# Performance work log

Hardware: AMD Instinct MI355X
Metric: run time of the kernel (lower is better)

The kernel has to match this reference:

```python
import jax, jax.numpy as jnp
import numpy as np

IN_DIMS = [16, 16, 16]
OUT_DIMS = [16, 16, 16]
RANKS = [1, 16, 16, 1]
BATCH = 1024


def setup_inputs() -> dict:
    key = jax.random.key(0)
    ks = jax.random.split(key, 1 + len(IN_DIMS))
    vector = jax.random.normal(ks[0], (BATCH, *IN_DIMS), dtype=jnp.float32)
    inp = {"vector": vector}
    for i in range(len(IN_DIMS)):
        shape = (RANKS[i], OUT_DIMS[i], IN_DIMS[i], RANKS[i + 1])
        scale = 1.0 / float(np.sqrt(RANKS[i] * IN_DIMS[i]))
        inp[f"core{i}"] = jax.random.normal(ks[1 + i], shape, dtype=jnp.float32) * scale
    return inp


def _tt_matvec(vector, cores):
    """y = M @ x where M is the TT/MPO matrix defined by `cores`.

    vector: (B, d_in_1, ..., d_in_d). Returns (B, d_out_1, ..., d_out_d).
    Mirrors TTMatrix.metric_projection exactly (output dims absorbed into batch).
    """
    bs0 = vector.shape[0]
    res = vector[:, None]  # (B, r0=1, d_in_1, ..., d_in_d)
    bs = bs0
    for core in cores:
        r, o, i, k = core.shape
        rem = res.shape[3:]  # remaining un-contracted input dims
        res_t = res.reshape(bs, r, i, -1)  # (bs, r, i, x)
        # contract rank-in and input dim: (r,o,i,k),(b,r,i,x) -> (b,k,o,x)
        new = jnp.einsum('roik,brix->bkox', core, res_t)
        new = jnp.transpose(new, (0, 2, 1, 3)).reshape(bs * o, k, *rem)
        bs = bs * o
        res = new
    res = jnp.squeeze(res, axis=-1)  # last rank is 1
    out_dims = [c.shape[1] for c in cores]
    return res.reshape(bs0, *out_dims)


def reference(vector, core0, core1, core2):
    return _tt_matvec(vector, (core0, core1, core2))
```

## Files before the change

kernel.cpp:

```cpp
#include <hip/hip_runtime.h>
#include <hip/hip_bf16.h>


typedef short bf16x8 __attribute__((ext_vector_type(8)));
typedef float f32x4 __attribute__((ext_vector_type(4)));

#define WS_A1_OFF 0
#define WS_A0_OFF 131072
#define WS_A2_OFF 147456
#define WS_NEEDED 155648

__device__ __forceinline__ unsigned short f2bf(float f) {
    union { float f; unsigned int u; } x; x.f = f;
    unsigned int u = x.u;
    u += 0x7fffu + ((u >> 16) & 1u);
    return (unsigned short)(u >> 16);
}

__device__ __forceinline__ unsigned int pk_bf16(float lo, float hi) {
    __hip_bfloat162 h = __float22bfloat162_rn(make_float2(lo, hi));
    unsigned int r;
    __builtin_memcpy(&r, &h, 4);
    return r;
}

__global__ void tt_repack(const float* __restrict__ c0,
                          const float* __restrict__ c1,
                          const float* __restrict__ c2,
                          unsigned short* __restrict__ ws) {
    int idx = blockIdx.x * 256 + threadIdx.x;
    if (idx < 8192) {
        int o2 = idx >> 9, ks = (idx >> 6) & 7, l = idx & 63;
        int k2 = l & 15;
        unsigned short* dst = ws + ((size_t)(o2 * 8 + ks) * 64 + l) * 8;
        #pragma unroll
        for (int j = 0; j < 8; ++j) {
            int k = ks * 32 + ((l >> 4) * 8) + j;
            dst[j] = f2bf(c1[(k & 15) * 4096 + o2 * 256 + (k >> 4) * 16 + k2]);
        }
    } else if (idx < 9216) {
        int t = idx - 8192;
        int o1 = t >> 6, l = t & 63;
        unsigned short* dst = ws + WS_A0_OFF / 2 + ((size_t)o1 * 64 + l) * 8;
        #pragma unroll
        for (int j = 0; j < 8; ++j) {
            int k = ((l >> 4) * 8) + j;
            float v = (l < 32) ? c0[o1 * 256 + k * 16 + (l & 15)] : 0.f;
            dst[j] = f2bf(v);
        }
    } else if (idx < 9728) {
        int t = idx - 9216;
        int ks = t >> 6, l = t & 63;
        unsigned short* dst = ws + WS_A2_OFF / 2 + ((size_t)ks * 64 + l) * 8;
        #pragma unroll
        for (int j = 0; j < 8; ++j) {
            int k = ks * 32 + ((l >> 4) * 8) + j;
            dst[j] = f2bf(c2[(k & 15) * 256 + (l & 15) * 16 + (k >> 4)]);
        }
    }
}

template <bool PACKED>
__global__ __launch_bounds__(512, 2) void tt_main(
    const float* __restrict__ vg, const float* __restrict__ c0,
    const float* __restrict__ c1, const float* __restrict__ c2,
    const unsigned short* __restrict__ ws, float* __restrict__ outg)
{
    __shared__ unsigned short T1[16384];
    __shared__ unsigned short T2[2][16384];

    const int b   = blockIdx.x;
    const int t   = threadIdx.x;
    const int w   = t >> 6;
    const int l   = t & 63;
    const int l15 = l & 15;
    const int lg  = l >> 4;
    const int mg  = w >> 1;
    const int ng  = w & 1;

    bf16x8 fb0[2];
    {
        const float* vb = vg + (size_t)b * 4096;
        #pragma unroll
        for (int nt = 0; nt < 2; ++nt) {
            bf16x8 f = {0, 0, 0, 0, 0, 0, 0, 0};
            if (l < 32) {
                int i2 = 2 * w + nt;
                const float* p = vb + (lg * 8) * 256 + i2 * 16 + l15;
                #pragma unroll
                for (int j = 0; j < 8; ++j) f[j] = (short)f2bf(p[j * 256]);
            }
            fb0[nt] = f;
        }
    }

    bf16x8 fa1p[32];
    if constexpr (PACKED) {
        const unsigned short* a1p = ws + (size_t)l * 8;
        #pragma unroll
        for (int rt = 0; rt < 4; ++rt)
            #pragma unroll
            for (int ks = 0; ks < 8; ++ks)
                fa1p[rt * 8 + ks] = *(const bf16x8*)(a1p + ((size_t)((4 * mg + rt) * 8 + ks)) * 512);
    } else {
        for (int rt = 0; rt < 4; ++rt)
            for (int ks = 0; ks < 8; ++ks) {
                int o2 = 4 * mg + rt;
                bf16x8 f;
                for (int j = 0; j < 8; ++j) {
                    int k = ks * 32 + lg * 8 + j;
                    f[j] = (short)f2bf(c1[(k & 15) * 4096 + o2 * 256 + (k >> 4) * 16 + l15]);
                }
                fa1p[rt * 8 + ks] = f;
            }
    }

    for (int nc = 0; nc < 4; ++nc) {
        unsigned short* T2c = T2[nc & 1];

        bf16x8 fa0p[4];
        if constexpr (PACKED) {
            #pragma unroll
            for (int mtl = 0; mtl < 4; ++mtl)
                fa0p[mtl] = *(const bf16x8*)(ws + WS_A0_OFF / 2 +
                                             ((size_t)(nc * 4 + mtl) * 64 + l) * 8);
        } else {
            for (int mtl = 0; mtl < 4; ++mtl) {
                bf16x8 f = {0, 0, 0, 0, 0, 0, 0, 0};
                if (l < 32) {
                    for (int j = 0; j < 8; ++j)
                        f[j] = (short)f2bf(c0[(nc * 4 + mtl) * 256 + (lg * 8 + j) * 16 + l15]);
                }
                fa0p[mtl] = f;
            }
        }

        #pragma unroll
        for (int mtl = 0; mtl < 4; ++mtl) {
            #pragma unroll
            for (int nt = 0; nt < 2; ++nt) {
                f32x4 z = {0.f, 0.f, 0.f, 0.f};
                f32x4 d = __builtin_amdgcn_mfma_f32_16x16x32_bf16(fa0p[mtl], fb0[nt], z, 0, 0, 0);
                const int i2 = 2 * w + nt;
                const int n  = mtl * 16 + l15;
                int byte = (n * 512 + (i2 * 16 + lg * 4) * 2) ^ ((l15 & 7) << 4);
                uint2 wv;
                wv.x = pk_bf16(d[0], d[1]);
                wv.y = pk_bf16(d[2], d[3]);
                *(uint2*)((char*)T1 + byte) = wv;
            }
        }
        __syncthreads();

        {
            f32x4 acc[4][2];
            #pragma unroll
            for (int rt = 0; rt < 4; ++rt)
                #pragma unroll
                for (int ntl = 0; ntl < 2; ++ntl) acc[rt][ntl] = (f32x4){0.f, 0.f, 0.f, 0.f};

            #pragma unroll
            for (int ks = 0; ks < 8; ++ks) {
                #pragma unroll
                for (int ntl = 0; ntl < 2; ++ntl) {
                    const int nt = 2 * ng + ntl;
                    int byte = ((nt * 16 + l15) * 512 + (ks * 32 + lg * 8) * 2) ^ ((l15 & 7) << 4);
                    bf16x8 fb = *(const bf16x8*)((char*)T1 + byte);
                    acc[0][ntl] = __builtin_amdgcn_mfma_f32_16x16x32_bf16(fa1p[0 * 8 + ks], fb, acc[0][ntl], 0, 0, 0);
                    acc[1][ntl] = __builtin_amdgcn_mfma_f32_16x16x32_bf16(fa1p[1 * 8 + ks], fb, acc[1][ntl], 0, 0, 0);
                    acc[2][ntl] = __builtin_amdgcn_mfma_f32_16x16x32_bf16(fa1p[2 * 8 + ks], fb, acc[2][ntl], 0, 0, 0);
                    acc[3][ntl] = __builtin_amdgcn_mfma_f32_16x16x32_bf16(fa1p[3 * 8 + ks], fb, acc[3][ntl], 0, 0, 0);
                }
            }
            #pragma unroll
            for (int rt = 0; rt < 4; ++rt) {
                const int o2 = 4 * mg + rt;
                #pragma unroll
                for (int ntl = 0; ntl < 2; ++ntl) {
                    const int nt = 2 * ng + ntl;
                    int byte = ((nt * 16 + o2) * 512 + (l15 * 16 + lg * 4) * 2) ^ ((o2 & 7) << 4);
                    uint2 wv;
                    wv.x = pk_bf16(acc[rt][ntl][0], acc[rt][ntl][1]);
                    wv.y = pk_bf16(acc[rt][ntl][2], acc[rt][ntl][3]);
                    *(uint2*)((char*)T2c + byte) = wv;
                }
            }
        }
        __syncthreads();

        if (w < 4) {
            bf16x8 fa2[8];
            if constexpr (PACKED) {
                #pragma unroll
                for (int ks = 0; ks < 8; ++ks)
                    fa2[ks] = *(const bf16x8*)(ws + WS_A2_OFF / 2 + ((size_t)ks * 64 + l) * 8);
            } else {
                for (int ks = 0; ks < 8; ++ks) {
                    bf16x8 f;
                    for (int j = 0; j < 8; ++j) {
                        int k = ks * 32 + lg * 8 + j;
                        f[j] = (short)f2bf(c2[(k & 15) * 256 + l15 * 16 + (k >> 4)]);
                    }
                    fa2[ks] = f;
                }
            }
            f32x4 a3a = {0.f, 0.f, 0.f, 0.f};
            f32x4 a3b = {0.f, 0.f, 0.f, 0.f};
            #pragma unroll
            for (int ks = 0; ks < 8; ks += 2) {
                int byte0 = ((w * 16 + l15) * 512 + ((ks + 0) * 32 + lg * 8) * 2) ^ ((l15 & 7) << 4);
                int byte1 = ((w * 16 + l15) * 512 + ((ks + 1) * 32 + lg * 8) * 2) ^ ((l15 & 7) << 4);
                bf16x8 fbA = *(const bf16x8*)((char*)T2c + byte0);
                bf16x8 fbB = *(const bf16x8*)((char*)T2c + byte1);
                a3a = __builtin_amdgcn_mfma_f32_16x16x32_bf16(fa2[ks],     fbA, a3a, 0, 0, 0);
                a3b = __builtin_amdgcn_mfma_f32_16x16x32_bf16(fa2[ks + 1], fbB, a3b, 0, 0, 0);
            }
            f32x4 acc3 = a3a + a3b;
            float* ob = outg + (size_t)b * 4096;
            *(f32x4*)(ob + (nc * 4 + w) * 256 + l15 * 16 + lg * 4) = acc3;
        }
    }
}

extern "C" void kernel_launch(void* const* d_in, const int* in_sizes, int n_in,
                              void* d_out, int out_size, void* d_ws, size_t ws_size,
                              hipStream_t stream) {
    const float* vg  = (const float*)d_in[0];
    const float* c0g = (const float*)d_in[1];
    const float* c1g = (const float*)d_in[2];
    const float* c2g = (const float*)d_in[3];
    float* outg = (float*)d_out;

    const int B = in_sizes[0] / 4096;
    const bool packed = (ws_size >= (size_t)WS_NEEDED) && (d_ws != nullptr);

    if (packed) {
        tt_repack<<<dim3(38), dim3(256), 0, stream>>>(c0g, c1g, c2g, (unsigned short*)d_ws);
        tt_main<true><<<dim3(B), dim3(512), 0, stream>>>(
            vg, c0g, c1g, c2g, (const unsigned short*)d_ws, outg);
    } else {
        tt_main<false><<<dim3(B), dim3(512), 0, stream>>>(
            vg, c0g, c1g, c2g, nullptr, outg);
    }
}
```

Measured before the change: 57.49 us.

## Fold cores 0 and 1 into a combined weight and batch four vectors per block

Adds a new path that precomputes the product of core0 and core1 into a 256x256-per-o1 bf16 weight matrix in workspace, then a main kernel that handles four batch elements per block. It runs one large GEMM per o1 against the staged input, with the core2 contraction for the previous o1 overlapped using double-buffered shared memory. This removes the separate first-stage contraction and the per-block T1 round trip, and spreads weight loads over four batch items. In exchange it needs about 2 MB of workspace, a heavier repack kernel, more weight traffic per block from L2, and it changes bf16 rounding because the fused weights are rounded once.

```diff
diff --git a/kernel.cpp b/kernel.cpp
--- a/kernel.cpp
+++ b/kernel.cpp
@@ -9,6 +9,9 @@
 #define WS_A0_OFF 131072
 #define WS_A2_OFF 147456
 #define WS_NEEDED 155648
+#define WS2_W12_OFF 0
+#define WS2_C2_OFF  2097152
+#define WS2_NEEDED  2105344
 
 __device__ __forceinline__ unsigned short f2bf(float f) {
     union { float f; unsigned int u; } x; x.f = f;
@@ -23,6 +26,174 @@
     __builtin_memcpy(&r, &h, 4);
     return r;
 }
+
+
+__global__ void tt_repack2(const float* __restrict__ c0,
+                           const float* __restrict__ c1,
+                           const float* __restrict__ c2,
+                           unsigned short* __restrict__ ws) {
+    if (blockIdx.x < 256) {
+        int idx = blockIdx.x * 512 + threadIdx.x;
+        int mt = idx >> 9, ks = (idx >> 6) & 7, l = idx & 63;
+        int o1 = mt >> 4, o2 = mt & 15;
+        int k2 = l & 15, lg = l >> 4;
+        int i1 = 2 * ks + (lg >> 1);
+        int i2b = (lg & 1) * 8;
+        float c0row[16];
+        #pragma unroll
+        for (int k1 = 0; k1 < 16; ++k1) c0row[k1] = c0[o1 * 256 + i1 * 16 + k1];
+        unsigned short* dst = ws + ((size_t)(mt * 8 + ks) * 64 + l) * 8;
+        #pragma unroll
+        for (int j = 0; j < 8; ++j) {
+            int i2 = i2b + j;
+            float s = 0.f;
+            #pragma unroll
+            for (int k1 = 0; k1 < 16; ++k1)
+                s += c0row[k1] * c1[k1 * 4096 + o2 * 256 + i2 * 16 + k2];
+            dst[j] = f2bf(s);
+        }
+    } else {
+        int t = threadIdx.x;
+        int ks = t >> 6, l = t & 63;
+        unsigned short* dst = ws + WS2_C2_OFF / 2 + ((size_t)ks * 64 + l) * 8;
+        #pragma unroll
+        for (int j = 0; j < 8; ++j) {
+            int k = ks * 32 + ((l >> 4) * 8) + j;
+            dst[j] = f2bf(c2[(k & 15) * 256 + (l & 15) * 16 + (k >> 4)]);
+        }
+    }
+}
+
+__global__ __launch_bounds__(512, 2) void tt_main2(
+    const float* __restrict__ vg, const unsigned short* __restrict__ ws,
+    float* __restrict__ outg)
+{
+    __shared__ unsigned short vS[16384];
+    __shared__ unsigned short T2[2][16384];
+
+    const int b0  = blockIdx.x * 4;
+    const int t   = threadIdx.x;
+    const int w   = t >> 6;
+    const int l   = t & 63;
+    const int l15 = l & 15;
+    const int lg  = l >> 4;
+
+    bf16x8 fa2[8];
+    #pragma unroll
+    for (int ks = 0; ks < 8; ++ks)
+        fa2[ks] = *(const bf16x8*)(ws + WS2_C2_OFF / 2 + ((size_t)ks * 64 + l) * 8);
+
+    {
+        const int bl  = t >> 7;
+        const int i3  = (t >> 3) & 15;
+        const int i1h = t & 7;
+        const float* vb = vg + (size_t)(b0 + bl) * 4096;
+        const int rowbyte = (bl * 16 + i3) * 512;
+        const int swz = (i3 & 7) << 4;
+        #pragma unroll
+        for (int q = 0; q < 4; ++q) {
+            const int i1  = 2 * i1h + (q >> 1);
+            const int i2b = (q & 1) * 8;
+            unsigned int pk[4];
+            #pragma unroll
+            for (int p = 0; p < 4; ++p) {
+                float lo = vb[i1 * 256 + (i2b + 2 * p)     * 16 + i3];
+                float hi = vb[i1 * 256 + (i2b + 2 * p + 1) * 16 + i3];
+                pk[p] = pk_bf16(lo, hi);
+            }
+            int byte = (rowbyte + (i1 * 16 + i2b) * 2) ^ swz;
+            *(uint4*)((char*)vS + byte) = make_uint4(pk[0], pk[1], pk[2], pk[3]);
+        }
+    }
+    __syncthreads();
+
+    const int o2a = w, o2b = w + 8;
+
+    int curr = 0;
+    for (int o1 = 0; o1 < 16; ++o1) {
+        bf16x8 fA0[8], fA1[8];
+        #pragma unroll
+        for (int ks = 0; ks < 8; ++ks) {
+            fA0[ks] = *(const bf16x8*)(ws + ((size_t)((o1 * 16 + o2a) * 8 + ks) * 64 + l) * 8);
+            fA1[ks] = *(const bf16x8*)(ws + ((size_t)((o1 * 16 + o2b) * 8 + ks) * 64 + l) * 8);
+        }
+
+        if (o1 > 0 && w < 4) {
+            const unsigned short* T2p = T2[curr ^ 1];
+            f32x4 a3a = {0.f, 0.f, 0.f, 0.f};
+            f32x4 a3b = {0.f, 0.f, 0.f, 0.f};
+            #pragma unroll
+            for (int ks3 = 0; ks3 < 8; ks3 += 2) {
+                const int i3A = 2 * ks3 + (lg >> 1);
+                const int i3B = i3A + 2;
+                const int k2b = (lg & 1) * 8;
+                int byteA = ((w * 16 + i3A) * 512 + (l15 * 16 + k2b) * 2) ^ ((i3A & 7) << 4);
+                int byteB = ((w * 16 + i3B) * 512 + (l15 * 16 + k2b) * 2) ^ ((i3B & 7) << 4);
+                bf16x8 fbA = *(const bf16x8*)((char*)T2p + byteA);
+                bf16x8 fbB = *(const bf16x8*)((char*)T2p + byteB);
+                a3a = __builtin_amdgcn_mfma_f32_16x16x32_bf16(fa2[ks3],     fbA, a3a, 0, 0, 0);
+                a3b = __builtin_amdgcn_mfma_f32_16x16x32_bf16(fa2[ks3 + 1], fbB, a3b, 0, 0, 0);
+            }
+            f32x4 acc3 = a3a + a3b;
+            *(f32x4*)(outg + (size_t)(b0 + w) * 4096 + (o1 - 1) * 256 + l15 * 16 + lg * 4) = acc3;
+        }
+
+        {
+            f32x4 acc[2][4];
+            #pragma unroll
+            for (int mi = 0; mi < 2; ++mi)
+                #pragma unroll
+                for (int nt = 0; nt < 4; ++nt) acc[mi][nt] = (f32x4){0.f, 0.f, 0.f, 0.f};
+
+            #pragma unroll
+            for (int ks = 0; ks < 8; ++ks) {
+                #pragma unroll
+                for (int nt = 0; nt < 4; ++nt) {
+                    int byte = ((nt * 16 + l15) * 512 + (ks * 32 + lg * 8) * 2) ^ ((l15 & 7) << 4);
+                    bf16x8 fb = *(const bf16x8*)((char*)vS + byte);
+                    acc[0][nt] = __builtin_amdgcn_mfma_f32_16x16x32_bf16(fA0[ks], fb, acc[0][nt], 0, 0, 0);
+                    acc[1][nt] = __builtin_amdgcn_mfma_f32_16x16x32_bf16(fA1[ks], fb, acc[1][nt], 0, 0, 0);
+                }
+            }
+            unsigned short* T2c = T2[curr];
+            #pragma unroll
+            for (int mi = 0; mi < 2; ++mi) {
+                const int o2 = mi ? o2b : o2a;
+                #pragma unroll
+                for (int nt = 0; nt < 4; ++nt) {
+                    int byte = ((nt * 16 + l15) * 512 + (o2 * 16 + lg * 4) * 2) ^ ((l15 & 7) << 4);
+                    uint2 wv;
+                    wv.x = pk_bf16(acc[mi][nt][0], acc[mi][nt][1]);
+                    wv.y = pk_bf16(acc[mi][nt][2], acc[mi][nt][3]);
+                    *(uint2*)((char*)T2c + byte) = wv;
+                }
+            }
+        }
+        __syncthreads();
+        curr ^= 1;
+    }
+
+    if (w < 4) {
+        const unsigned short* T2p = T2[curr ^ 1];
+        f32x4 a3a = {0.f, 0.f, 0.f, 0.f};
+        f32x4 a3b = {0.f, 0.f, 0.f, 0.f};
+        #pragma unroll
+        for (int ks3 = 0; ks3 < 8; ks3 += 2) {
+            const int i3A = 2 * ks3 + (lg >> 1);
+            const int i3B = i3A + 2;
+            const int k2b = (lg & 1) * 8;
+            int byteA = ((w * 16 + i3A) * 512 + (l15 * 16 + k2b) * 2) ^ ((i3A & 7) << 4);
+            int byteB = ((w * 16 + i3B) * 512 + (l15 * 16 + k2b) * 2) ^ ((i3B & 7) << 4);
+            bf16x8 fbA = *(const bf16x8*)((char*)T2p + byteA);
+            bf16x8 fbB = *(const bf16x8*)((char*)T2p + byteB);
+            a3a = __builtin_amdgcn_mfma_f32_16x16x32_bf16(fa2[ks3],     fbA, a3a, 0, 0, 0);
+            a3b = __builtin_amdgcn_mfma_f32_16x16x32_bf16(fa2[ks3 + 1], fbB, a3b, 0, 0, 0);
+        }
+        f32x4 acc3 = a3a + a3b;
+        *(f32x4*)(outg + (size_t)(b0 + w) * 4096 + 15 * 256 + l15 * 16 + lg * 4) = acc3;
+    }
+}
+
 
 __global__ void tt_repack(const float* __restrict__ c0,
                           const float* __restrict__ c1,
@@ -69,14 +240,10 @@
     __shared__ unsigned short T1[16384];
     __shared__ unsigned short T2[2][16384];
 
-    const int b   = blockIdx.x;
-    const int t   = threadIdx.x;
-    const int w   = t >> 6;
-    const int l   = t & 63;
-    const int l15 = l & 15;
-    const int lg  = l >> 4;
-    const int mg  = w >> 1;
-    const int ng  = w & 1;
+    const int b = blockIdx.x;
+    const int t = threadIdx.x;
+    const int w = t >> 6, l = t & 63, l15 = l & 15, lg = l >> 4;
+    const int mg = w >> 1, ng = w & 1;
 
     bf16x8 fb0[2];
     {
@@ -93,7 +260,6 @@
             fb0[nt] = f;
         }
     }
-
     bf16x8 fa1p[32];
     if constexpr (PACKED) {
         const unsigned short* a1p = ws + (size_t)l * 8;
@@ -117,7 +283,6 @@
 
     for (int nc = 0; nc < 4; ++nc) {
         unsigned short* T2c = T2[nc & 1];
-
         bf16x8 fa0p[4];
         if constexpr (PACKED) {
             #pragma unroll
@@ -134,7 +299,6 @@
                 fa0p[mtl] = f;
             }
         }
-
         #pragma unroll
         for (int mtl = 0; mtl < 4; ++mtl) {
             #pragma unroll
@@ -151,14 +315,12 @@
             }
         }
         __syncthreads();
-
         {
             f32x4 acc[4][2];
             #pragma unroll
             for (int rt = 0; rt < 4; ++rt)
                 #pragma unroll
                 for (int ntl = 0; ntl < 2; ++ntl) acc[rt][ntl] = (f32x4){0.f, 0.f, 0.f, 0.f};
-
             #pragma unroll
             for (int ks = 0; ks < 8; ++ks) {
                 #pragma unroll
@@ -187,7 +349,6 @@
             }
         }
         __syncthreads();
-
         if (w < 4) {
             bf16x8 fa2[8];
             if constexpr (PACKED) {
@@ -232,9 +393,13 @@
     float* outg = (float*)d_out;
 
     const int B = in_sizes[0] / 4096;
-    const bool packed = (ws_size >= (size_t)WS_NEEDED) && (d_ws != nullptr);
-
-    if (packed) {
+
+    if (ws_size >= (size_t)WS2_NEEDED && d_ws != nullptr && (B % 4) == 0) {
+        tt_repack2<<<dim3(257), dim3(512), 0, stream>>>(
+            c0g, c1g, c2g, (unsigned short*)d_ws);
+        tt_main2<<<dim3(B / 4), dim3(512), 0, stream>>>(
+            vg, (const unsigned short*)d_ws, outg);
+    } else if (ws_size >= (size_t)WS_NEEDED && d_ws != nullptr) {
         tt_repack<<<dim3(38), dim3(256), 0, stream>>>(c0g, c1g, c2g, (unsigned short*)d_ws);
         tt_main<true><<<dim3(B), dim3(512), 0, stream>>>(
             vg, c0g, c1g, c2g, (const unsigned short*)d_ws, outg);
```

Result: faster. 54.18 us (-5.8%).
